# Kernel tuning notes

Measured on AMD Instinct MI355X. Metric: run time of the kernel, lower is better.

## Reference

```python
import jax, jax.numpy as jnp
import numpy as np

N = 8_388_608  # total flattened scalar parameters across the model
K = 64         # VQ codebook size (dim = 1 -> scalar quantization)
W_STD = 0.02   # typical init std for MLP weights


def setup_inputs() -> dict:
    key = jax.random.key(0)
    k1, k2 = jax.random.split(key)
    weights = jax.random.normal(k1, (N,), dtype=jnp.float32) * W_STD
    codebook = jax.random.normal(k2, (K,), dtype=jnp.float32) * W_STD
    return {"weights": weights, "codebook": codebook}


def reference(weights, codebook):
    # VectorQuantize with dim=1: squared L2 distance of each scalar weight to
    # each scalar code, argmin, replace with nearest code (cdist+argmin+lookup).
    # dist[n, k] = (w_n - c_k)^2  -> [N, K]
    dist = (weights[:, None] - codebook[None, :]) ** 2
    idx = jnp.argmin(dist, axis=1)           # [N] nearest code index
    quantized = codebook[idx]                # [N] codebook replacement
    # straight-through estimator (as in vector-quantize-pytorch)
    return weights + jax.lax.stop_gradient(quantized - weights)
```

## Files before the change

### kernel.cpp

```cpp
#include <hip/hip_runtime.h>


#define VQ_K 64
#define NB   1024
#define NW   (NB / 4)
#define TPB  256
#define SEG  2
#define ITERS 4
#define BLK_F4 (TPB * SEG * ITERS)

__device__ __forceinline__ unsigned bytesum(unsigned x) {
    return (x + (x >> 8) + (x >> 16) + (x >> 24)) & 0xFFu;
}

__device__ __forceinline__ int vq_key(float x, float inv, float nlo) {
    float t = fmaf(x, inv, nlo);
    t = fminf(fmaxf(t, 0.0f), (float)(NB - 1));
    return (int)t;
}

__global__ __launch_bounds__(TPB, 4) void vq_kernel(
    const float* __restrict__ w,
    const float* __restrict__ cb,
    float* __restrict__ out,
    int n4)
{
    __shared__ float  C[VQ_K];
    __shared__ float  S[VQ_K + 4];
    __shared__ float4 T[NB];
    __shared__ unsigned H[NW];
    __shared__ unsigned Hs[NW];

    const int tid = threadIdx.x;
    const float INF = __builtin_inff();
    const float NANF = __uint_as_float(0x7fc00000u);

    if (tid < VQ_K) C[tid] = cb[tid];
    H[tid] = 0u;
    __syncthreads();

    if (tid < VQ_K) {
        const float c = C[tid];
        int rank = 0;
#pragma unroll
        for (int j = 0; j < VQ_K; ++j) {
            const float cj = C[j];
            rank += (cj < c || (cj == c && j < tid)) ? 1 : 0;
        }
        S[rank + 1] = c;
    }
    if (tid == 0) S[0] = INF;
    if (tid >= VQ_K + 1 && tid <= VQ_K + 3) S[tid] = INF;
    __syncthreads();

    const float lo  = S[1];
    const float hi  = S[VQ_K];
    const float inv = (hi > lo) ? ((float)NB / (hi - lo)) : 0.0f;
    const float nlo = -lo * inv;

    if (tid < VQ_K) {
        const int k = vq_key(S[tid + 1], inv, nlo);
        atomicAdd(&H[k >> 2], 1u << ((k & 3) * 8));
    }
    __syncthreads();

    if (tid < 64) {
        const unsigned w0 = H[4 * tid], w1 = H[4 * tid + 1];
        const unsigned w2 = H[4 * tid + 2], w3 = H[4 * tid + 3];
        const int s0 = (int)bytesum(w0), s1 = (int)bytesum(w1);
        const int s2 = (int)bytesum(w2), s3 = (int)bytesum(w3);
        const int tot = s0 + s1 + s2 + s3;
        int acc = tot;
#pragma unroll
        for (int d = 1; d < 64; d <<= 1) {
            int u = __shfl_up(acc, d, 64);
            if (tid >= d) acc += u;
        }
        const int base = acc - tot;
        Hs[4 * tid]     = (unsigned)base;
        Hs[4 * tid + 1] = (unsigned)(base + s0);
        Hs[4 * tid + 2] = (unsigned)(base + s0 + s1);
        Hs[4 * tid + 3] = (unsigned)(base + s0 + s1 + s2);
    }
    __syncthreads();

#pragma unroll
    for (int j = 0; j < 4; ++j) {
        const int b = tid + j * TPB;
        const unsigned hw = H[b >> 2];
        const int sh = (b & 3) * 8;
        const int h = (int)((hw >> sh) & 0xFFu);
        const unsigned below = hw & ((sh == 0) ? 0u : ((1u << sh) - 1u));
        const int p0 = (int)Hs[b >> 2] + (int)bytesum(below);
        float4 ent;
        if (h >= 3) ent = make_float4(NANF, NANF, NANF, NANF);
        else        ent = make_float4(S[p0], S[p0 + 1], S[p0 + 2], S[p0 + 3]);
        T[b] = ent;
    }
    __syncthreads();

    const float4* in4 = reinterpret_cast<const float4*>(w);
    float4* out4 = reinterpret_cast<float4*>(out);
    const int blk_base = blockIdx.x * BLK_F4;

#pragma unroll 1
    for (int it = 0; it < ITERS; ++it) {
        const int base4 = blk_base + it * (TPB * SEG) + tid;

        float4 x[SEG];
#pragma unroll
        for (int s = 0; s < SEG; ++s) x[s] = in4[base4 + s * TPB];

        int key[SEG][4];
#pragma unroll
        for (int s = 0; s < SEG; ++s) {
            const float* e = &x[s].x;
#pragma unroll
            for (int j = 0; j < 4; ++j) key[s][j] = vq_key(e[j], inv, nlo);
        }

        float4 ent[SEG][4];
#pragma unroll
        for (int s = 0; s < SEG; ++s)
#pragma unroll
            for (int j = 0; j < 4; ++j) ent[s][j] = T[key[s][j]];

        float4 r[SEG];
        unsigned badmask = 0u;
#pragma unroll
        for (int s = 0; s < SEG; ++s) {
            const float* e = &x[s].x;
            float* ro = &r[s].x;
#pragma unroll
            for (int j = 0; j < 4; ++j) {
                const float wv = e[j];
                const float4 en = ent[s][j];
                const bool s1 = (en.y <= wv);
                const bool s2 = (en.z <= wv);
                const float cl = s2 ? en.z : (s1 ? en.y : en.x);
                const float cr = s2 ? en.w : (s1 ? en.z : en.y);
                const float dl = wv - cl, dr = wv - cr;
                const float dl2 = dl * dl, dr2 = dr * dr;
                const bool rlt = (dr2 < dl2);
                ro[j] = rlt ? cr : cl;
                const bool bad = !rlt && !(dl2 < dr2) && (cl != cr);
                badmask |= bad ? (1u << (s * 4 + j)) : 0u;
            }
        }

        if (__any(badmask != 0u)) {
            if (badmask != 0u) {
#pragma unroll
                for (int s = 0; s < SEG; ++s) {
                    const float* e = &x[s].x;
                    float* ro = &r[s].x;
#pragma unroll
                    for (int j = 0; j < 4; ++j) {
                        if (badmask & (1u << (s * 4 + j))) {
                            const float wv = e[j];
                            float c0 = C[0], d0 = wv - c0;
                            float bd = d0 * d0, bv = c0;
#pragma unroll 1
                            for (int kk = 1; kk < VQ_K; ++kk) {
                                float cc = C[kk], d = wv - cc, dd = d * d;
                                bool lt = dd < bd;
                                bd = lt ? dd : bd;
                                bv = lt ? cc : bv;
                            }
                            ro[j] = bv;
                        }
                    }
                }
            }
        }

#pragma unroll
        for (int s = 0; s < SEG; ++s) out4[base4 + s * TPB] = r[s];
    }
}

__global__ void vq_tail_kernel(const float* __restrict__ w,
                               const float* __restrict__ cb,
                               float* __restrict__ out, int start, int n) {
    int i = start + blockIdx.x * blockDim.x + threadIdx.x;
    if (i >= n) return;
    float wx = w[i];
    float c0 = cb[0], d0 = wx - c0;
    float bd = d0 * d0, bv = c0;
#pragma unroll
    for (int k = 1; k < VQ_K; ++k) {
        float c = cb[k], d = wx - c, dd = d * d;
        bool lt = dd < bd;
        bd = lt ? dd : bd;
        bv = lt ? c : bv;
    }
    out[i] = bv;
}

extern "C" void kernel_launch(void* const* d_in, const int* in_sizes, int n_in,
                              void* d_out, int out_size, void* d_ws, size_t ws_size,
                              hipStream_t stream) {
    const float* w  = (const float*)d_in[0];
    const float* cb = (const float*)d_in[1];
    float* out = (float*)d_out;
    const int n  = in_sizes[0];
    const int n4 = n / 4;

    const int grid = n4 / BLK_F4;
    if (grid > 0) {
        vq_kernel<<<grid, TPB, 0, stream>>>(w, cb, out, n4);
    }
    const int done = grid * BLK_F4 * 4;
    if (done < n) {
        const int rem = n - done;
        vq_tail_kernel<<<(rem + TPB - 1) / TPB, TPB, 0, stream>>>(w, cb, out, done, n);
    }
}
```

Before: 19.09 us.

## Software-pipeline loads with single segment, higher occupancy, nontemporal stores

Cuts per-iteration work from two float4 segments to one and prefetches the next iteration's input before processing the current one. Launch bounds rise from 4 to 8 blocks per CU to allow more waves, and output writes use nontemporal stores to avoid polluting cache. Blocks now cover half as much data, so twice as many blocks each rebuild the shared-memory lookup table, which adds setup overhead.

Result: faster. 18.24 us (-4.4%).

```diff
diff --git a/kernel.cpp b/kernel.cpp
--- a/kernel.cpp
+++ b/kernel.cpp
@@ -5,9 +5,11 @@
 #define NB   1024
 #define NW   (NB / 4)
 #define TPB  256
-#define SEG  2
+#define SEG  1
 #define ITERS 4
 #define BLK_F4 (TPB * SEG * ITERS)
+
+typedef float f32x4n __attribute__((ext_vector_type(4)));
 
 __device__ __forceinline__ unsigned bytesum(unsigned x) {
     return (x + (x >> 8) + (x >> 16) + (x >> 24)) & 0xFFu;
@@ -19,7 +21,7 @@
     return (int)t;
 }
 
-__global__ __launch_bounds__(TPB, 4) void vq_kernel(
+__global__ __launch_bounds__(TPB, 8) void vq_kernel(
     const float* __restrict__ w,
     const float* __restrict__ cb,
     float* __restrict__ out,
@@ -100,82 +102,74 @@
     __syncthreads();
 
     const float4* in4 = reinterpret_cast<const float4*>(w);
-    float4* out4 = reinterpret_cast<float4*>(out);
+    f32x4n* out4 = reinterpret_cast<f32x4n*>(out);
     const int blk_base = blockIdx.x * BLK_F4;
+
+    float4 x = in4[blk_base + tid];
 
 #pragma unroll 1
     for (int it = 0; it < ITERS; ++it) {
-        const int base4 = blk_base + it * (TPB * SEG) + tid;
-
-        float4 x[SEG];
-#pragma unroll
-        for (int s = 0; s < SEG; ++s) x[s] = in4[base4 + s * TPB];
-
-        int key[SEG][4];
-#pragma unroll
-        for (int s = 0; s < SEG; ++s) {
-            const float* e = &x[s].x;
-#pragma unroll
-            for (int j = 0; j < 4; ++j) key[s][j] = vq_key(e[j], inv, nlo);
-        }
-
-        float4 ent[SEG][4];
-#pragma unroll
-        for (int s = 0; s < SEG; ++s)
-#pragma unroll
-            for (int j = 0; j < 4; ++j) ent[s][j] = T[key[s][j]];
-
-        float4 r[SEG];
+        const int base4 = blk_base + it * TPB + tid;
+
+        float4 xn;
+        if (it + 1 < ITERS) xn = in4[base4 + TPB];
+
+        const float* e = &x.x;
+        int key[4];
+#pragma unroll
+        for (int j = 0; j < 4; ++j) key[j] = vq_key(e[j], inv, nlo);
+
+        float4 ent[4];
+#pragma unroll
+        for (int j = 0; j < 4; ++j) ent[j] = T[key[j]];
+
+        float4 r;
+        float* ro = &r.x;
         unsigned badmask = 0u;
 #pragma unroll
-        for (int s = 0; s < SEG; ++s) {
-            const float* e = &x[s].x;
-            float* ro = &r[s].x;
-#pragma unroll
-            for (int j = 0; j < 4; ++j) {
-                const float wv = e[j];
-                const float4 en = ent[s][j];
-                const bool s1 = (en.y <= wv);
-                const bool s2 = (en.z <= wv);
-                const float cl = s2 ? en.z : (s1 ? en.y : en.x);
-                const float cr = s2 ? en.w : (s1 ? en.z : en.y);
-                const float dl = wv - cl, dr = wv - cr;
-                const float dl2 = dl * dl, dr2 = dr * dr;
-                const bool rlt = (dr2 < dl2);
-                ro[j] = rlt ? cr : cl;
-                const bool bad = !rlt && !(dl2 < dr2) && (cl != cr);
-                badmask |= bad ? (1u << (s * 4 + j)) : 0u;
-            }
+        for (int j = 0; j < 4; ++j) {
+            const float wv = e[j];
+            const float4 en = ent[j];
+            const bool s1 = (en.y <= wv);
+            const bool s2 = (en.z <= wv);
+            const float cl = s2 ? en.z : (s1 ? en.y : en.x);
+            const float cr = s2 ? en.w : (s1 ? en.z : en.y);
+            const float dl = wv - cl, dr = wv - cr;
+            const float dl2 = dl * dl, dr2 = dr * dr;
+            const bool rlt = (dr2 < dl2);
+            ro[j] = rlt ? cr : cl;
+            const bool bad = !rlt && !(dl2 < dr2) && (cl != cr);
+            badmask |= bad ? (1u << j) : 0u;
         }
 
         if (__any(badmask != 0u)) {
             if (badmask != 0u) {
 #pragma unroll
-                for (int s = 0; s < SEG; ++s) {
-                    const float* e = &x[s].x;
-                    float* ro = &r[s].x;
-#pragma unroll
-                    for (int j = 0; j < 4; ++j) {
-                        if (badmask & (1u << (s * 4 + j))) {
-                            const float wv = e[j];
-                            float c0 = C[0], d0 = wv - c0;
-                            float bd = d0 * d0, bv = c0;
+                for (int j = 0; j < 4; ++j) {
+                    if (badmask & (1u << j)) {
+                        const float wv = e[j];
+                        float c0 = C[0], d0 = wv - c0;
+                        float bd = d0 * d0, bv = c0;
 #pragma unroll 1
-                            for (int kk = 1; kk < VQ_K; ++kk) {
-                                float cc = C[kk], d = wv - cc, dd = d * d;
-                                bool lt = dd < bd;
-                                bd = lt ? dd : bd;
-                                bv = lt ? cc : bv;
-                            }
-                            ro[j] = bv;
+                        for (int kk = 1; kk < VQ_K; ++kk) {
+                            float cc = C[kk], d = wv - cc, dd = d * d;
+                            bool lt = dd < bd;
+                            bd = lt ? dd : bd;
+                            bv = lt ? cc : bv;
                         }
+                        ro[j] = bv;
                     }
                 }
             }
         }
 
-#pragma unroll
-        for (int s = 0; s < SEG; ++s) out4[base4 + s * TPB] = r[s];
+        {
+            f32x4n rv;
+            rv.x = r.x; rv.y = r.y; rv.z = r.z; rv.w = r.w;
+            __builtin_nontemporal_store(rv, &out4[base4]);
+        }
+
+        x = xn;
     }
 }
 
```
